# Kernel optimization log

Measured on AMD Instinct MI355X. Metric: run time of the kernel, lower is better.

The kernel has to match this reference:

```python
import jax, jax.numpy as jnp
import numpy as np

T, B, I, H = 512, 64, 512, 512

def setup_inputs() -> dict:
    key = jax.random.key(0)
    k1, k2, k3 = jax.random.split(key, 3)
    # scale weights to keep tanh out of deep saturation
    return {
        "input": jax.random.normal(k1, (T, B, I), dtype=jnp.float32),
        "w_ih": jax.random.normal(k2, (H, I), dtype=jnp.float32) / np.sqrt(I),
        "w_hh": jax.random.normal(k3, (H, H), dtype=jnp.float32) / np.sqrt(H),
    }

def reference(input, w_ih, w_hh):
    # vanilla tanh RNN: h_t = tanh(x_t @ w_ih^T + h_{t-1} @ w_hh^T)
    batch = input.shape[1]
    h0 = jnp.zeros((batch, w_hh.shape[0]), dtype=input.dtype)

    def step(h_prev, x):
        h = jnp.tanh(x @ w_ih.T + h_prev @ w_hh.T)
        return h, h

    h_last, h_all = jax.lax.scan(step, h0, input)
    return h_all, h_last
```

## Files before the change

kernel.cpp:

```cpp
#include <hip/hip_runtime.h>
#include <cmath>

#define T_STEPS 512
#define BATCH   64
#define ISZ     512
#define HSZ     512
#define EXN     32768

__device__ __forceinline__ void ex_store(unsigned long long* w, float h, unsigned tag) {
    union { float f; unsigned u; } c; c.f = h;
    const unsigned long long v = ((unsigned long long)tag << 32) | (unsigned long long)c.u;
    __hip_atomic_store(w, v, __ATOMIC_RELAXED, __HIP_MEMORY_SCOPE_AGENT);
}

#define KEEP4(v) asm volatile("" : "+v"((v).x), "+v"((v).y), "+v"((v).z), "+v"((v).w))

__device__ __forceinline__ float dot_fold_pick(const float4 (&W)[2][8],
                                               const float4* __restrict__ src,
                                               int parbase4, int kseg,
                                               int jxr, int br) {
    float A00 = 0.f, A01 = 0.f, A10 = 0.f, A11 = 0.f;
    const float4* s0 = src + parbase4 + kseg * 9;
    const float4* s1 = s0 + 144;
    #pragma unroll
    for (int i = 0; i < 8; ++i) {
        const float4 h0 = s0[i];
        const float4 h1 = s1[i];
        A00 = fmaf(W[0][i].x, h0.x, A00); A00 = fmaf(W[0][i].y, h0.y, A00);
        A00 = fmaf(W[0][i].z, h0.z, A00); A00 = fmaf(W[0][i].w, h0.w, A00);
        A01 = fmaf(W[0][i].x, h1.x, A01); A01 = fmaf(W[0][i].y, h1.y, A01);
        A01 = fmaf(W[0][i].z, h1.z, A01); A01 = fmaf(W[0][i].w, h1.w, A01);
        A10 = fmaf(W[1][i].x, h0.x, A10); A10 = fmaf(W[1][i].y, h0.y, A10);
        A10 = fmaf(W[1][i].z, h0.z, A10); A10 = fmaf(W[1][i].w, h0.w, A10);
        A11 = fmaf(W[1][i].x, h1.x, A11); A11 = fmaf(W[1][i].y, h1.y, A11);
        A11 = fmaf(W[1][i].w, h1.w, A11); A11 = fmaf(W[1][i].z, h1.z, A11);
    }
    #pragma unroll
    for (int d = 1; d < 16; d <<= 1) {
        A00 += __shfl_xor(A00, d, 64);
        A01 += __shfl_xor(A01, d, 64);
        A10 += __shfl_xor(A10, d, 64);
        A11 += __shfl_xor(A11, d, 64);
    }
    const float a0 = br ? A01 : A00;
    const float a1 = br ? A11 : A10;
    return jxr ? a1 : a0;
}

__global__ __launch_bounds__(512, 2) void rnn_fused(const float* __restrict__ x,
                                                    const float* __restrict__ wih,
                                                    const float* __restrict__ whh,
                                                    float* __restrict__ out,
                                                    unsigned long long* __restrict__ ex) {
    __shared__ __align__(16) float hls[2304];
    __shared__ __align__(16) float xss[2304];
    const float4* hl4 = (const float4*)hls;
    const float4* xs4 = (const float4*)xss;

    const int tid  = threadIdx.x;
    const int bid  = blockIdx.x;
    const int xcd  = bid & 7;
    const int ib   = bid >> 3;
    const int p    = xcd * 4 + (ib & 3);
    const int g    = ib >> 2;
    const int kseg = tid & 15;
    const int jg   = tid >> 4;
    const int jb   = g * 64 + jg * 2;

    float4 wh[2][8], wi[2][8];
    #pragma unroll
    for (int jx = 0; jx < 2; ++jx) {
        const float* hr = whh + (size_t)(jb + jx) * HSZ + kseg * 32;
        const float* ir = wih + (size_t)(jb + jx) * ISZ + kseg * 32;
        #pragma unroll
        for (int i = 0; i < 8; ++i) {
            wh[jx][i] = *(const float4*)(hr + 4 * i);
            wi[jx][i] = *(const float4*)(ir + 4 * i);
        }
    }
    #pragma unroll
    for (int jx = 0; jx < 2; ++jx)
        #pragma unroll
        for (int i = 0; i < 8; ++i) { KEEP4(wh[jx][i]); KEEP4(wi[jx][i]); }

    unsigned long long* exw0 = ex + (size_t)(2 * p + 0) * 512 + tid;
    unsigned long long* exw1 = ex + (size_t)(2 * p + 1) * 512 + tid;

    const int whf = ((tid >> 5) * 9 + ((tid >> 2) & 7)) * 4 + (tid & 3);

    const int bx = tid >> 8;
    const int io = (tid & 255) * 2;
    const int xf = ((bx * 16 + (io >> 5)) * 9 + ((io >> 2) & 7)) * 4 + (io & 3);
    const float* xsrc = x + (size_t)(2 * p + bx) * ISZ + io;

    const int jxr  = kseg >> 1;
    const int br   = kseg & 1;
    const int outj = jb + (jxr & 1);
    const int outb = 2 * p + br;
    float* outp = out + (size_t)outb * HSZ + outj;
    unsigned long long* exself = ex + (size_t)outb * 512 + outj;

    {
        const float2 v = *(const float2*)xsrc;
        *(float2*)&xss[xf] = v;
    }
    __syncthreads();
    float xwv = dot_fold_pick(wi, xs4, 0, kseg, jxr, br);

    for (int t = 0; t < T_STEPS; ++t) {
        const int  parh  = (t & 1) * 288;
        const bool havex = (t < T_STEPS - 1);

        float2 xv;
        if (havex) xv = *(const float2*)(xsrc + (size_t)(t + 1) * (BATCH * ISZ));

        if (t > 0) {
            const size_t soff = (size_t)((t - 1) & 1) * EXN;
            unsigned long long v0 = __hip_atomic_load(exw0 + soff, __ATOMIC_RELAXED,
                                                      __HIP_MEMORY_SCOPE_AGENT);
            unsigned long long v1 = __hip_atomic_load(exw1 + soff, __ATOMIC_RELAXED,
                                                      __HIP_MEMORY_SCOPE_AGENT);
            while ((unsigned)(v0 >> 32) != (unsigned)t ||
                   (unsigned)(v1 >> 32) != (unsigned)t) {
                __builtin_amdgcn_s_sleep(1);
                v0 = __hip_atomic_load(exw0 + soff, __ATOMIC_RELAXED,
                                       __HIP_MEMORY_SCOPE_AGENT);
                v1 = __hip_atomic_load(exw1 + soff, __ATOMIC_RELAXED,
                                       __HIP_MEMORY_SCOPE_AGENT);
            }
            union { unsigned u; float f; } c0, c1;
            c0.u = (unsigned)v0; c1.u = (unsigned)v1;
            hls[parh * 4 + whf]       = c0.f;
            hls[parh * 4 + 576 + whf] = c1.f;
        }
        if (havex) *(float2*)&xss[((t + 1) & 1) * 1152 + xf] = xv;
        __syncthreads();

        float acc = 0.f;
        if (t > 0)
            acc = dot_fold_pick(wh, hl4, parh, kseg, jxr, br);

        if (kseg < 4) {
            const float a2 = acc + xwv;
            const float e  = __expf(2.f * a2);
            const float hv = 1.f - 2.f / (e + 1.f);
            outp[(size_t)t * (BATCH * HSZ)] = hv;
            if (havex)
                ex_store(exself + (size_t)(t & 1) * EXN, hv, (unsigned)(t + 1));
            else
                out[(size_t)T_STEPS * BATCH * HSZ + (size_t)outb * HSZ + outj] = hv;
        }

        if (havex)
            xwv = dot_fold_pick(wi, xs4, ((t + 1) & 1) * 288, kseg, jxr, br);
    }
}

extern "C" void kernel_launch(void* const* d_in, const int* in_sizes, int n_in,
                              void* d_out, int out_size, void* d_ws, size_t ws_size,
                              hipStream_t stream) {
    (void)in_sizes; (void)n_in; (void)out_size; (void)ws_size;
    const float* x   = (const float*)d_in[0];
    const float* wih = (const float*)d_in[1];
    const float* whh = (const float*)d_in[2];
    float*       out = (float*)d_out;
    unsigned long long* ex = (unsigned long long*)d_ws;

    (void)hipMemsetAsync(d_ws, 0, 2 * EXN * sizeof(unsigned long long), stream);

    hipLaunchKernelGGL(rnn_fused, dim3(256), dim3(512), 0, stream,
                       x, wih, whh, out, ex);
}
```

Measured before the change: 1.125 ms.

## Split reduction across 32 lanes with 4 rows each and a transpose-style shuffle fold

Each thread now handles 4 output rows over a 16-element k-slice, with 32 lanes per row group instead of 16 lanes for 2 rows. The final cross-lane reduction becomes a butterfly that exchanges partial sums, so the 8 results are spread across lanes instead of every lane reducing all four accumulators fully. This cuts shuffle count per step and raises the number of lanes doing tanh/output work from 4 to 8 per group. The shared-memory padding changes from 9-float4 to 5-float4 strides to match the new slices, and the weights are pinned in registers with a dummy zero add instead of an empty asm barrier.

```diff
diff --git a/kernel.cpp b/kernel.cpp
--- a/kernel.cpp
+++ b/kernel.cpp
@@ -13,38 +13,48 @@
     __hip_atomic_store(w, v, __ATOMIC_RELAXED, __HIP_MEMORY_SCOPE_AGENT);
 }
 
-#define KEEP4(v) asm volatile("" : "+v"((v).x), "+v"((v).y), "+v"((v).z), "+v"((v).w))
-
-__device__ __forceinline__ float dot_fold_pick(const float4 (&W)[2][8],
-                                               const float4* __restrict__ src,
-                                               int parbase4, int kseg,
-                                               int jxr, int br) {
-    float A00 = 0.f, A01 = 0.f, A10 = 0.f, A11 = 0.f;
-    const float4* s0 = src + parbase4 + kseg * 9;
-    const float4* s1 = s0 + 144;
+__device__ __forceinline__ float dot16_fold(const float4 (&W)[4][4],
+                                            const float4* __restrict__ src,
+                                            int parbase4, int kseg) {
+    const float4* s0 = src + parbase4 + kseg * 5;
+    const float4* s1 = s0 + 160;
+    float A0 = 0.f, A1 = 0.f, A2 = 0.f, A3 = 0.f;
+    float B0 = 0.f, B1 = 0.f, B2 = 0.f, B3 = 0.f;
     #pragma unroll
-    for (int i = 0; i < 8; ++i) {
+    for (int i = 0; i < 4; ++i) {
         const float4 h0 = s0[i];
         const float4 h1 = s1[i];
-        A00 = fmaf(W[0][i].x, h0.x, A00); A00 = fmaf(W[0][i].y, h0.y, A00);
-        A00 = fmaf(W[0][i].z, h0.z, A00); A00 = fmaf(W[0][i].w, h0.w, A00);
-        A01 = fmaf(W[0][i].x, h1.x, A01); A01 = fmaf(W[0][i].y, h1.y, A01);
-        A01 = fmaf(W[0][i].z, h1.z, A01); A01 = fmaf(W[0][i].w, h1.w, A01);
-        A10 = fmaf(W[1][i].x, h0.x, A10); A10 = fmaf(W[1][i].y, h0.y, A10);
-        A10 = fmaf(W[1][i].z, h0.z, A10); A10 = fmaf(W[1][i].w, h0.w, A10);
-        A11 = fmaf(W[1][i].x, h1.x, A11); A11 = fmaf(W[1][i].y, h1.y, A11);
-        A11 = fmaf(W[1][i].w, h1.w, A11); A11 = fmaf(W[1][i].z, h1.z, A11);
+        const float4 w0 = W[0][i], w1 = W[1][i], w2 = W[2][i], w3 = W[3][i];
+        A0 = fmaf(w0.x, h0.x, A0); A0 = fmaf(w0.y, h0.y, A0);
+        A0 = fmaf(w0.z, h0.z, A0); A0 = fmaf(w0.w, h0.w, A0);
+        A1 = fmaf(w1.x, h0.x, A1); A1 = fmaf(w1.y, h0.y, A1);
+        A1 = fmaf(w1.z, h0.z, A1); A1 = fmaf(w1.w, h0.w, A1);
+        A2 = fmaf(w2.x, h0.x, A2); A2 = fmaf(w2.y, h0.y, A2);
+        A2 = fmaf(w2.z, h0.z, A2); A2 = fmaf(w2.w, h0.w, A2);
+        A3 = fmaf(w3.x, h0.x, A3); A3 = fmaf(w3.y, h0.y, A3);
+        A3 = fmaf(w3.z, h0.z, A3); A3 = fmaf(w3.w, h0.w, A3);
+        B0 = fmaf(w0.x, h1.x, B0); B0 = fmaf(w0.y, h1.y, B0);
+        B0 = fmaf(w0.z, h1.z, B0); B0 = fmaf(w0.w, h1.w, B0);
+        B1 = fmaf(w1.x, h1.x, B1); B1 = fmaf(w1.y, h1.y, B1);
+        B1 = fmaf(w1.z, h1.z, B1); B1 = fmaf(w1.w, h1.w, B1);
+        B2 = fmaf(w2.x, h1.x, B2); B2 = fmaf(w2.y, h1.y, B2);
+        B2 = fmaf(w2.z, h1.z, B2); B2 = fmaf(w2.w, h1.w, B2);
+        B3 = fmaf(w3.x, h1.x, B3); B3 = fmaf(w3.y, h1.y, B3);
+        B3 = fmaf(w3.z, h1.z, B3); B3 = fmaf(w3.w, h1.w, B3);
     }
-    #pragma unroll
-    for (int d = 1; d < 16; d <<= 1) {
-        A00 += __shfl_xor(A00, d, 64);
-        A01 += __shfl_xor(A01, d, 64);
-        A10 += __shfl_xor(A10, d, 64);
-        A11 += __shfl_xor(A11, d, 64);
-    }
-    const float a0 = br ? A01 : A00;
-    const float a1 = br ? A11 : A10;
-    return jxr ? a1 : a0;
+    const bool sb0 = (kseg & 1) != 0;
+    const bool sb1 = (kseg & 2) != 0;
+    const bool sb2 = (kseg & 4) != 0;
+    const float u0 = (sb0 ? B0 : A0) + __shfl_xor(sb0 ? A0 : B0, 1, 64);
+    const float u1 = (sb0 ? B1 : A1) + __shfl_xor(sb0 ? A1 : B1, 1, 64);
+    const float u2 = (sb0 ? B2 : A2) + __shfl_xor(sb0 ? A2 : B2, 1, 64);
+    const float u3 = (sb0 ? B3 : A3) + __shfl_xor(sb0 ? A3 : B3, 1, 64);
+    const float w01 = (sb1 ? u1 : u0) + __shfl_xor(sb1 ? u0 : u1, 2, 64);
+    const float w23 = (sb1 ? u3 : u2) + __shfl_xor(sb1 ? u2 : u3, 2, 64);
+    float z = (sb2 ? w23 : w01) + __shfl_xor(sb2 ? w01 : w23, 4, 64);
+    z += __shfl_xor(z, 8, 64);
+    z += __shfl_xor(z, 16, 64);
+    return z;
 }
 
 __global__ __launch_bounds__(512, 2) void rnn_fused(const float* __restrict__ x,
@@ -52,8 +62,8 @@
                                                     const float* __restrict__ whh,
                                                     float* __restrict__ out,
                                                     unsigned long long* __restrict__ ex) {
-    __shared__ __align__(16) float hls[2304];
-    __shared__ __align__(16) float xss[2304];
+    __shared__ __align__(16) float hls[2560];
+    __shared__ __align__(16) float xss[2560];
     const float4* hl4 = (const float4*)hls;
     const float4* xs4 = (const float4*)xss;
 
@@ -63,39 +73,44 @@
     const int ib   = bid >> 3;
     const int p    = xcd * 4 + (ib & 3);
     const int g    = ib >> 2;
-    const int kseg = tid & 15;
-    const int jg   = tid >> 4;
-    const int jb   = g * 64 + jg * 2;
+    const int kseg = tid & 31;
+    const int jg   = tid >> 5;
+    const int jb   = g * 64 + jg * 4;
 
-    float4 wh[2][8], wi[2][8];
+    float4 wh[4][4], wi[4][4];
     #pragma unroll
-    for (int jx = 0; jx < 2; ++jx) {
-        const float* hr = whh + (size_t)(jb + jx) * HSZ + kseg * 32;
-        const float* ir = wih + (size_t)(jb + jx) * ISZ + kseg * 32;
+    for (int r = 0; r < 4; ++r) {
+        const float* hr = whh + (size_t)(jb + r) * HSZ + kseg * 16;
+        const float* ir = wih + (size_t)(jb + r) * ISZ + kseg * 16;
         #pragma unroll
-        for (int i = 0; i < 8; ++i) {
-            wh[jx][i] = *(const float4*)(hr + 4 * i);
-            wi[jx][i] = *(const float4*)(ir + 4 * i);
+        for (int i = 0; i < 4; ++i) {
+            wh[r][i] = *(const float4*)(hr + 4 * i);
+            wi[r][i] = *(const float4*)(ir + 4 * i);
         }
     }
+    float oz;
+    asm volatile("v_mov_b32 %0, 0" : "=v"(oz));
     #pragma unroll
-    for (int jx = 0; jx < 2; ++jx)
+    for (int r = 0; r < 4; ++r)
         #pragma unroll
-        for (int i = 0; i < 8; ++i) { KEEP4(wh[jx][i]); KEEP4(wi[jx][i]); }
+        for (int i = 0; i < 4; ++i) {
+            wh[r][i].x += oz; wh[r][i].y += oz; wh[r][i].z += oz; wh[r][i].w += oz;
+            wi[r][i].x += oz; wi[r][i].y += oz; wi[r][i].z += oz; wi[r][i].w += oz;
+        }
 
     unsigned long long* exw0 = ex + (size_t)(2 * p + 0) * 512 + tid;
     unsigned long long* exw1 = ex + (size_t)(2 * p + 1) * 512 + tid;
 
-    const int whf = ((tid >> 5) * 9 + ((tid >> 2) & 7)) * 4 + (tid & 3);
+    const int whf = (tid >> 4) * 20 + ((tid >> 2) & 3) * 4 + (tid & 3);
 
     const int bx = tid >> 8;
     const int io = (tid & 255) * 2;
-    const int xf = ((bx * 16 + (io >> 5)) * 9 + ((io >> 2) & 7)) * 4 + (io & 3);
+    const int xf = bx * 640 + (io >> 4) * 20 + ((io >> 2) & 3) * 4 + (io & 3);
     const float* xsrc = x + (size_t)(2 * p + bx) * ISZ + io;
 
-    const int jxr  = kseg >> 1;
+    const int row  = ((kseg >> 1) & 1) + 2 * ((kseg >> 2) & 1);
     const int br   = kseg & 1;
-    const int outj = jb + (jxr & 1);
+    const int outj = jb + row;
     const int outb = 2 * p + br;
     float* outp = out + (size_t)outb * HSZ + outj;
     unsigned long long* exself = ex + (size_t)outb * 512 + outj;
@@ -105,10 +120,10 @@
         *(float2*)&xss[xf] = v;
     }
     __syncthreads();
-    float xwv = dot_fold_pick(wi, xs4, 0, kseg, jxr, br);
+    float xwv = dot16_fold(wi, xs4, 0, kseg);
 
     for (int t = 0; t < T_STEPS; ++t) {
-        const int  parh  = (t & 1) * 288;
+        const int  parh4 = (t & 1) * 320;
         const bool havex = (t < T_STEPS - 1);
 
         float2 xv;
@@ -130,17 +145,17 @@
             }
             union { unsigned u; float f; } c0, c1;
             c0.u = (unsigned)v0; c1.u = (unsigned)v1;
-            hls[parh * 4 + whf]       = c0.f;
-            hls[parh * 4 + 576 + whf] = c1.f;
+            hls[parh4 * 4 + whf]       = c0.f;
+            hls[parh4 * 4 + 640 + whf] = c1.f;
         }
-        if (havex) *(float2*)&xss[((t + 1) & 1) * 1152 + xf] = xv;
+        if (havex) *(float2*)&xss[((t + 1) & 1) * 1280 + xf] = xv;
         __syncthreads();
 
         float acc = 0.f;
         if (t > 0)
-            acc = dot_fold_pick(wh, hl4, parh, kseg, jxr, br);
+            acc = dot16_fold(wh, hl4, parh4, kseg);
 
-        if (kseg < 4) {
+        if (kseg < 8) {
             const float a2 = acc + xwv;
             const float e  = __expf(2.f * a2);
             const float hv = 1.f - 2.f / (e + 1.f);
@@ -152,7 +167,7 @@
         }
 
         if (havex)
-            xwv = dot_fold_pick(wi, xs4, ((t + 1) & 1) * 288, kseg, jxr, br);
+            xwv = dot16_fold(wi, xs4, ((t + 1) & 1) * 320, kseg);
     }
 }
 
```

Measured after the change: 1.038 ms. 1.08x faster.
